# Kernel optimization log

Hardware: AMD Instinct MI355X
Metric: run time of the kernel (lower is better)

## Reference

```python
import jax, jax.numpy as jnp
import numpy as np

TEMP = 0.2
L_MAIN, L_VIEW, L_SUP, L_UNSUP = 1.0, 1.0, 1.0, 0.2
N, D, V, P, NEG, U = 100000, 256, 3, 1024, 1024, 2048


def setup_inputs() -> dict:
    key = jax.random.key(0)
    ks = jax.random.split(key, 8)
    fused_logit = jax.random.normal(ks[0], (N,), dtype=jnp.float32)
    view_logits = jax.random.normal(ks[1], (V, N), dtype=jnp.float32)
    proj = jax.random.normal(ks[2], (V, N, D), dtype=jnp.float32)
    proj = proj / jnp.linalg.norm(proj, axis=-1, keepdims=True)  # 'already normalized'
    labels = jax.random.randint(ks[3], (N,), 0, 2).astype(jnp.float32)
    train_mask = jax.random.randint(ks[4], (N,), 0, 2).astype(bool)
    train_pos_idx = jax.random.randint(ks[5], (P,), 0, N)
    train_neg_idx = jax.random.randint(ks[6], (NEG,), 0, N)
    unlabeled_idx = jax.random.randint(ks[7], (U,), 0, N)  # len == max_unsup_samples -> no subsampling
    return dict(fused_logit=fused_logit, view_logits=view_logits, proj=proj,
                labels=labels, train_mask=train_mask, train_pos_idx=train_pos_idx,
                train_neg_idx=train_neg_idx, unlabeled_idx=unlabeled_idx)


def _masked_bce(logits, labels, mask):
    # BCEWithLogitsLoss mean over masked elements (stable formulation)
    bce = jnp.maximum(logits, 0) - logits * labels + jnp.log1p(jnp.exp(-jnp.abs(logits)))
    mf = mask.astype(logits.dtype)
    return jnp.sum(bce * mf) / jnp.maximum(jnp.sum(mf), 1.0)


def _sup_contrastive(proj, pos_idx, neg_idx, temp):
    lab_idx = jnp.concatenate([pos_idx, neg_idx])
    node_labels = jnp.concatenate([jnp.ones(pos_idx.shape[0]), jnp.zeros(neg_idx.shape[0])])
    L = lab_idx.shape[0]
    Vv = proj.shape[0]
    z = proj[:, lab_idx, :].transpose(1, 0, 2)          # [L, V, D]
    zf = z.reshape(L * Vv, -1)                           # [L*V, D]
    sim = (zf @ zf.T) / temp                             # [L*V, L*V]
    sim = sim - jax.lax.stop_gradient(sim.max(axis=1, keepdims=True))
    es = jnp.exp(sim)
    node = jnp.repeat(jnp.arange(L), Vv)
    view = jnp.tile(jnp.arange(Vv), L)
    flab = jnp.repeat(node_labels, Vv)
    sn = node[:, None] == node[None, :]
    sv = view[:, None] == view[None, :]
    sl = flab[:, None] == flab[None, :]
    eye = jnp.eye(L * Vv, dtype=bool)
    pos_m = ((sn & ~sv) | (~sn & sl)) & ~eye
    neg_m = (~sn) & (~sl) & ~eye
    den_m = pos_m | neg_m
    denom = jnp.sum(es * den_m.astype(es.dtype), axis=1) + 1e-12
    posf = pos_m.astype(es.dtype)
    log_prob = -jnp.log((es * posf + 1e-12) / denom[:, None])
    pos_count = pos_m.sum(axis=1)
    loss_per_anchor = jnp.sum(log_prob * posf, axis=1) / (pos_count.astype(es.dtype) + 1e-12)
    valid = ((pos_count > 0) & (den_m.sum(axis=1) > 0)).astype(es.dtype)
    return jnp.sum(loss_per_anchor * valid) / jnp.maximum(jnp.sum(valid), 1.0)


def _unsup_consistency(proj, unl_idx, temp):
    # Vectorized form of the double python loop: full cosine-sim matrix with
    # masked denominator (all but self) and positives = same node, other views.
    Vv = proj.shape[0]
    z = proj[:, unl_idx, :].transpose(1, 0, 2)           # [U, V, D]
    Uu = z.shape[0]
    M = Uu * Vv
    zf = z.reshape(M, -1)
    zn = zf / (jnp.linalg.norm(zf, axis=1, keepdims=True) + 1e-8)
    es = jnp.exp((zn @ zn.T) / temp)                     # [M, M]
    denom = es.sum(axis=1) - jnp.diag(es) + 1e-12        # exclude self
    node = jnp.repeat(jnp.arange(Uu), Vv)
    view = jnp.tile(jnp.arange(Vv), Uu)
    pos_m = (node[:, None] == node[None, :]) & (view[:, None] != view[None, :])
    posf = pos_m.astype(es.dtype)
    log_prob = -jnp.log(es / denom[:, None])
    per_anchor = jnp.sum(log_prob * posf, axis=1) / (Vv - 1)
    return jnp.mean(per_anchor)


def reference(fused_logit, view_logits, proj, labels, train_mask,
              train_pos_idx, train_neg_idx, unlabeled_idx):
    main_loss = _masked_bce(fused_logit, labels, train_mask)
    view_loss = jnp.mean(jax.vmap(lambda lg: _masked_bce(lg, labels, train_mask))(view_logits))
    sup_loss = _sup_contrastive(proj, train_pos_idx, train_neg_idx, TEMP)
    unsup_loss = _unsup_consistency(proj, unlabeled_idx, TEMP)
    total = L_MAIN * main_loss + L_VIEW * view_loss + L_SUP * sup_loss + L_UNSUP * unsup_loss
    return jnp.stack([total, main_loss, view_loss, sup_loss, unsup_loss])
```

## Files before the change

### kernel.cpp

```cpp
#include <hip/hip_runtime.h>
#include <math.h>

typedef short short8 __attribute__((ext_vector_type(8)));
typedef float floatx4 __attribute__((ext_vector_type(4)));

#define TEMP_INV 5.0f
#define W_UNSUP 0.2f
#define NB_BCE 256
#define NSPLIT 8

static __device__ __forceinline__ unsigned short f2bf(float f) {
  unsigned int u = __float_as_uint(f);
  u += 0x7FFFu + ((u >> 16) & 1u);
  return (unsigned short)(u >> 16);
}

__device__ __forceinline__ float block_sum256(float v) {
  __shared__ float sh[4];
  for (int m = 1; m <= 32; m <<= 1) v += __shfl_xor(v, m);
  __syncthreads();
  if ((threadIdx.x & 63) == 0) sh[threadIdx.x >> 6] = v;
  __syncthreads();
  return sh[0] + sh[1] + sh[2] + sh[3];
}

__global__ void detect_kernel(const unsigned int* __restrict__ w, int nw, int* __restrict__ flag) {
  __shared__ int s_int, s_flt;
  if (threadIdx.x == 0) { s_int = 1; s_flt = 1; }
  __syncthreads();
  for (int i = threadIdx.x; i < nw; i += blockDim.x) {
    unsigned int x = w[i];
    if (x != 0u && x != 1u) s_int = 0;
    if (x != 0u && x != 0x3F800000u) s_flt = 0;
  }
  __syncthreads();
  if (threadIdx.x == 0) *flag = s_int ? 0 : (s_flt ? 1 : 2);
}

__global__ __launch_bounds__(256) void bce_kernel(
    const float* __restrict__ fused, const float* __restrict__ viewl,
    const float* __restrict__ labels, const void* __restrict__ maskp,
    const int* __restrict__ flagp, float* __restrict__ partials, int N, int V) {
  const int flag = *flagp;
  float cnt = 0.f, sm = 0.f;
  float sv[8];
  for (int v = 0; v < 8; v++) sv[v] = 0.f;
  const int Vc = V > 8 ? 8 : V;
  for (int i = blockIdx.x * blockDim.x + threadIdx.x; i < N; i += gridDim.x * blockDim.x) {
    bool m;
    if (flag == 0)      m = ((const int*)maskp)[i] != 0;
    else if (flag == 1) m = ((const float*)maskp)[i] != 0.0f;
    else                m = ((const unsigned char*)maskp)[i] != 0;
    if (!m) continue;
    float y = labels[i];
    cnt += 1.0f;
    float x = fused[i];
    sm += fmaxf(x, 0.f) - x * y + log1pf(__expf(-fabsf(x)));
    for (int v = 0; v < Vc; v++) {
      float xv = viewl[(size_t)v * N + i];
      sv[v] += fmaxf(xv, 0.f) - xv * y + log1pf(__expf(-fabsf(xv)));
    }
  }
  float tot = block_sum256(cnt);
  if (threadIdx.x == 0) partials[blockIdx.x * 16 + 0] = tot;
  tot = block_sum256(sm);
  if (threadIdx.x == 0) partials[blockIdx.x * 16 + 1] = tot;
  for (int v = 0; v < Vc; v++) {
    tot = block_sum256(sv[v]);
    if (threadIdx.x == 0) partials[blockIdx.x * 16 + 2 + v] = tot;
  }
}

__global__ __launch_bounds__(256) void gather_kernel(
    const float* __restrict__ proj, const int* __restrict__ pos_idx,
    const int* __restrict__ neg_idx, const int* __restrict__ unl_idx,
    unsigned short* __restrict__ zsup, unsigned short* __restrict__ zuns,
    float* __restrict__ dsup, float* __restrict__ duns,
    float* __restrict__ Esup, float* __restrict__ Bsup,
    float* __restrict__ Euns, float* __restrict__ Buns,
    int N, int D, int V, int P, int Msup, int Muns) {
  const int prob = blockIdx.y;
  const int M = prob ? Muns : Msup;
  const int r0 = blockIdx.x * 8;
  const int t = threadIdx.x;
  if (t < 8) {
    int rz = r0 + t;
    if (rz < M) {
      if (prob) { Euns[rz] = 0.f; Buns[rz] = 0.f; }
      else      { Esup[rz] = 0.f; Bsup[rz] = 0.f; }
    }
  }
  const int sub = t >> 5, ln = t & 31;
  const int r = r0 + sub;
  if (r >= M) return;
  const int l = r / V, v = r - l * V;
  const int idx = prob ? unl_idx[l] : (l < P ? pos_idx[l] : neg_idx[l - P]);
  const float* src = proj + ((size_t)v * N + (size_t)idx) * D + ln * 8;
  floatx4 p0 = *(const floatx4*)(src);
  floatx4 p1 = *(const floatx4*)(src + 4);
  float s = 0.f;
#pragma unroll
  for (int k = 0; k < 4; k++) s += p0[k] * p0[k] + p1[k] * p1[k];
  for (int m = 1; m <= 16; m <<= 1) s += __shfl_xor(s, m);
  const float n2 = s;
  float sc = 1.0f, dval = n2 * TEMP_INV;
  if (prob) {
    sc = 1.0f / (sqrtf(n2) + 1e-8f);
    dval = n2 * sc * sc * TEMP_INV;
  }
  short8 vv;
#pragma unroll
  for (int k = 0; k < 4; k++) {
    vv[k]     = (short)f2bf(p0[k] * sc);
    vv[k + 4] = (short)f2bf(p1[k] * sc);
  }
  unsigned short* zd = prob ? zuns : zsup;
  *(short8*)(zd + (size_t)r * 256 + ln * 8) = vv;
  if (ln == 0) (prob ? duns : dsup)[r] = dval;
}

__global__ __launch_bounds__(256) void sim_kernel(
    const unsigned short* __restrict__ zsup, const unsigned short* __restrict__ zuns,
    float* __restrict__ Esup, float* __restrict__ Bsup,
    float* __restrict__ Euns, float* __restrict__ Buns,
    int Msup, int Muns, int PV, int V, int nsSup, int nsUns) {
  const int prob = blockIdx.y;
  const unsigned short* __restrict__ z = prob ? zuns : zsup;
  float* __restrict__ Ep = prob ? Euns : Esup;
  float* __restrict__ Bp = prob ? Buns : Bsup;
  const int M = prob ? Muns : Msup;
  const int ns = prob ? nsUns : nsSup;

  const int si = blockIdx.x / NSPLIT;
  const int s  = blockIdx.x - si * NSPLIT;
  if (si >= ns) return;

  const int R0 = si * 64;
  const int tid = threadIdx.x;
  const int wave = tid >> 6;
  const int wr = wave >> 1, wc = wave & 1;
  const int q = (tid >> 4) & 3;
  const int n16 = tid & 15;

  __shared__ __align__(16) unsigned short lds[64 * 264];

  short8 a[2][8];
#pragma unroll
  for (int m = 0; m < 2; m++) {
    int row = R0 + wr * 32 + m * 16 + n16;
    if (row >= M) row = M - 1;
    const unsigned short* zr = z + (size_t)row * 256 + q * 8;
#pragma unroll
    for (int ks = 0; ks < 8; ks++) a[m][ks] = *(const short8*)(zr + ks * 32);
  }

  int bs[2][4], be[2][4];
#pragma unroll
  for (int m = 0; m < 2; m++)
#pragma unroll
    for (int r = 0; r < 4; r++) {
      int row = R0 + wr * 32 + m * 16 + q * 4 + r;
      if (row >= M) row = M - 1;
      if (prob == 0) { bs[m][r] = row < PV ? 0 : PV; be[m][r] = row < PV ? PV : M; }
      else           { int b0 = (row / V) * V; bs[m][r] = b0; be[m][r] = b0 + V; }
    }

  float er0[4] = {0, 0, 0, 0}, er1[4] = {0, 0, 0, 0};
  float br0[4] = {0, 0, 0, 0}, br1[4] = {0, 0, 0, 0};

  for (int tj = si + s; tj < ns; tj += NSPLIT) {
    const int C0 = tj * 64;
    __syncthreads();
#pragma unroll
    for (int cc = 0; cc < 8; cc++) {
      int chunk = cc * 256 + tid;
      int rrow = chunk >> 5;
      int off = (chunk & 31) * 8;
      int gcol = C0 + rrow;
      short8 vv = {0, 0, 0, 0, 0, 0, 0, 0};
      if (gcol < M) vv = *(const short8*)(z + (size_t)gcol * 256 + off);
      *(short8*)(&lds[rrow * 264 + off]) = vv;
    }
    __syncthreads();

    floatx4 acc00 = {0.f, 0.f, 0.f, 0.f}, acc01 = {0.f, 0.f, 0.f, 0.f};
    floatx4 acc10 = {0.f, 0.f, 0.f, 0.f}, acc11 = {0.f, 0.f, 0.f, 0.f};
#pragma unroll
    for (int ks = 0; ks < 8; ks++) {
      const unsigned short* bp = &lds[(wc * 32 + n16) * 264 + q * 8 + ks * 32];
      short8 b0 = *(const short8*)bp;
      short8 b1 = *(const short8*)(bp + 16 * 264);
      acc00 = __builtin_amdgcn_mfma_f32_16x16x32_bf16(a[0][ks], b0, acc00, 0, 0, 0);
      acc01 = __builtin_amdgcn_mfma_f32_16x16x32_bf16(a[0][ks], b1, acc01, 0, 0, 0);
      acc10 = __builtin_amdgcn_mfma_f32_16x16x32_bf16(a[1][ks], b0, acc10, 0, 0, 0);
      acc11 = __builtin_amdgcn_mfma_f32_16x16x32_bf16(a[1][ks], b1, acc11, 0, 0, 0);
    }

    float ec0 = 0.f, ec1 = 0.f, bc0 = 0.f, bc1 = 0.f;
    const int j0 = C0 + wc * 32 + n16;
    const int j1 = j0 + 16;

#define EPI(ACC, MM, JN, ECOL, BCOL, ERA, BRA)                        \
  _Pragma("unroll")                                                   \
  for (int r = 0; r < 4; r++) {                                       \
    int row = R0 + wr * 32 + MM * 16 + q * 4 + r;                     \
    float tv = ACC[r] * TEMP_INV;                                     \
    bool valid = (row < M) && (JN < M);                               \
    float e = valid ? __expf(tv - 5.0f) : 0.0f;                       \
    float bv = (valid && JN >= bs[MM][r] && JN < be[MM][r]) ? tv : 0.0f; \
    ERA[r] += e; BRA[r] += bv; ECOL += e; BCOL += bv;                 \
  }
    EPI(acc00, 0, j0, ec0, bc0, er0, br0)
    EPI(acc01, 0, j1, ec1, bc1, er0, br0)
    EPI(acc10, 1, j0, ec0, bc0, er1, br1)
    EPI(acc11, 1, j1, ec1, bc1, er1, br1)
#undef EPI

    if (tj != si) {
      float e = ec0, b = bc0;
      e += __shfl_xor(e, 16); e += __shfl_xor(e, 32);
      b += __shfl_xor(b, 16); b += __shfl_xor(b, 32);
      if (q == 0 && j0 < M) { atomicAdd(&Ep[j0], e); atomicAdd(&Bp[j0], b); }
      e = ec1; b = bc1;
      e += __shfl_xor(e, 16); e += __shfl_xor(e, 32);
      b += __shfl_xor(b, 16); b += __shfl_xor(b, 32);
      if (q == 0 && j1 < M) { atomicAdd(&Ep[j1], e); atomicAdd(&Bp[j1], b); }
    }
  }

#pragma unroll
  for (int mr = 0; mr < 8; mr++) {
    const int m = mr >> 2, r = mr & 3;
    float e = m ? er1[r] : er0[r];
    float b = m ? br1[r] : br0[r];
    for (int msk = 1; msk <= 8; msk <<= 1) { e += __shfl_xor(e, msk); b += __shfl_xor(b, msk); }
    int row = R0 + wr * 32 + m * 16 + q * 4 + r;
    if (n16 == 0 && row < M) {
      atomicAdd(&Ep[row], e);
      atomicAdd(&Bp[row], b);
    }
  }
}

__global__ __launch_bounds__(256) void finalize_kernel(
    const float* __restrict__ partials,
    const float* __restrict__ Esup, const float* __restrict__ Bsup, const float* __restrict__ dsup,
    const float* __restrict__ Euns, const float* __restrict__ Buns, const float* __restrict__ duns,
    int Msup, int Muns, int PV, int P, int NEG, int V, float* __restrict__ out) {
  const int t = threadIdx.x;
  float cnt = 0.f, sm = 0.f, sv[8];
  for (int v = 0; v < 8; v++) sv[v] = 0.f;
  const int Vc = V > 8 ? 8 : V;
  for (int b = t; b < NB_BCE; b += 256) {
    cnt += partials[b * 16 + 0];
    sm  += partials[b * 16 + 1];
    for (int v = 0; v < Vc; v++) sv[v] += partials[b * 16 + 2 + v];
  }
  cnt = block_sum256(cnt);
  sm = block_sum256(sm);
  float svt = 0.f;
  for (int v = 0; v < Vc; v++) svt += block_sum256(sv[v]);
  const float denomC = fmaxf(cnt, 1.0f);
  const float main_loss = sm / denomC;
  const float view_loss = (svt / denomC) / (float)V;

  float ssup = 0.f;
  for (int row = t; row < Msup; row += 256) {
    float E = Esup[row], B = Bsup[row];
    float d = dsup[row];
    float dn = E - __expf(d - 5.0f);
    float cl = (row < PV) ? (float)P : (float)NEG;
    float pc = (float)(V - 1) + (cl - 1.0f) * (float)V;
    ssup += logf(dn) + 5.0f - (B - d) / pc;
  }
  ssup = block_sum256(ssup);
  const float sup_loss = ssup / (float)Msup;

  float suns = 0.f;
  for (int row = t; row < Muns; row += 256) {
    float E = Euns[row], B = Buns[row];
    float d = duns[row];
    float dn = E - __expf(d - 5.0f);
    suns += logf(dn) + 5.0f - (B - d) / (float)(V - 1);
  }
  suns = block_sum256(suns);
  const float unsup_loss = suns / (float)Muns;

  if (t == 0) {
    float total = main_loss + view_loss + sup_loss + W_UNSUP * unsup_loss;
    out[0] = total;
    out[1] = main_loss;
    out[2] = view_loss;
    out[3] = sup_loss;
    out[4] = unsup_loss;
  }
}

extern "C" void kernel_launch(void* const* d_in, const int* in_sizes, int n_in,
                              void* d_out, int out_size, void* d_ws, size_t ws_size,
                              hipStream_t stream) {
  const float* fused  = (const float*)d_in[0];
  const float* viewl  = (const float*)d_in[1];
  const float* proj   = (const float*)d_in[2];
  const float* labels = (const float*)d_in[3];
  const void*  maskp  = d_in[4];
  const int* pos_idx  = (const int*)d_in[5];
  const int* neg_idx  = (const int*)d_in[6];
  const int* unl_idx  = (const int*)d_in[7];

  const int N = in_sizes[0];
  const int V = in_sizes[1] / N;
  const int D = in_sizes[2] / in_sizes[1];
  const int P = in_sizes[5];
  const int NEG = in_sizes[6];
  const int U = in_sizes[7];
  const int L = P + NEG;
  const int Msup = L * V;
  const int Muns = U * V;
  const int PV = P * V;

  char* ws = (char*)d_ws;
  size_t off = 0;
  auto alloc = [&](size_t bytes) { size_t o = off; off += (bytes + 255) & ~(size_t)255; return o; };
  const size_t o_flag = alloc(4);
  const size_t o_part = alloc((size_t)NB_BCE * 16 * 4);
  const size_t o_zsup = alloc((size_t)Msup * D * 2);
  const size_t o_zuns = alloc((size_t)Muns * D * 2);
  const size_t o_dsup = alloc((size_t)Msup * 4);
  const size_t o_duns = alloc((size_t)Muns * 4);
  const size_t o_Esup = alloc((size_t)Msup * 4);
  const size_t o_Bsup = alloc((size_t)Msup * 4);
  const size_t o_Euns = alloc((size_t)Muns * 4);
  const size_t o_Buns = alloc((size_t)Muns * 4);

  int* flag = (int*)(ws + o_flag);
  float* partials = (float*)(ws + o_part);
  unsigned short* zsup = (unsigned short*)(ws + o_zsup);
  unsigned short* zuns = (unsigned short*)(ws + o_zuns);
  float* dsup = (float*)(ws + o_dsup);
  float* duns = (float*)(ws + o_duns);
  float* Esup = (float*)(ws + o_Esup);
  float* Bsup = (float*)(ws + o_Bsup);
  float* Euns = (float*)(ws + o_Euns);
  float* Buns = (float*)(ws + o_Buns);

  int nw = N / 4 < 256 ? N / 4 : 256;
  detect_kernel<<<1, 256, 0, stream>>>((const unsigned int*)maskp, nw, flag);
  bce_kernel<<<NB_BCE, 256, 0, stream>>>(fused, viewl, labels, maskp, flag, partials, N, V);

  const int Mmax = Msup > Muns ? Msup : Muns;
  dim3 ggrid((Mmax + 7) / 8, 2);
  gather_kernel<<<ggrid, 256, 0, stream>>>(proj, pos_idx, neg_idx, unl_idx,
                                           zsup, zuns, dsup, duns,
                                           Esup, Bsup, Euns, Buns,
                                           N, D, V, P, Msup, Muns);

  const int nsS = (Msup + 63) / 64;
  const int nsU = (Muns + 63) / 64;
  const int nsMax = nsS > nsU ? nsS : nsU;
  dim3 sgrid(nsMax * NSPLIT, 2);
  sim_kernel<<<sgrid, 256, 0, stream>>>(zsup, zuns, Esup, Bsup, Euns, Buns,
                                        Msup, Muns, PV, V, nsS, nsU);

  finalize_kernel<<<1, 256, 0, stream>>>(partials, Esup, Bsup, dsup, Euns, Buns, duns,
                                         Msup, Muns, PV, P, NEG, V, (float*)d_out);
}
```

Baseline: 463.4 us.

## Prefetch next sim tile into registers and fold mask detection into BCE kernel

The sim kernel now loads the next 64-column tile of z into registers while the current tile is written to LDS and consumed, so global load latency overlaps the MFMA work. The separate single-block detect kernel is removed; every BCE block now redoes the mask-dtype detection itself, saving one launch and the serial dependency. The cost is extra register pressure from the eight prefetch vectors, and redundant detection reads in each BCE block.

```diff
diff --git a/kernel.cpp b/kernel.cpp
--- a/kernel.cpp
+++ b/kernel.cpp
@@ -24,29 +24,33 @@
   return sh[0] + sh[1] + sh[2] + sh[3];
 }
 
-__global__ void detect_kernel(const unsigned int* __restrict__ w, int nw, int* __restrict__ flag) {
-  __shared__ int s_int, s_flt;
-  if (threadIdx.x == 0) { s_int = 1; s_flt = 1; }
-  __syncthreads();
-  for (int i = threadIdx.x; i < nw; i += blockDim.x) {
-    unsigned int x = w[i];
-    if (x != 0u && x != 1u) s_int = 0;
-    if (x != 0u && x != 0x3F800000u) s_flt = 0;
-  }
-  __syncthreads();
-  if (threadIdx.x == 0) *flag = s_int ? 0 : (s_flt ? 1 : 2);
-}
-
 __global__ __launch_bounds__(256) void bce_kernel(
     const float* __restrict__ fused, const float* __restrict__ viewl,
     const float* __restrict__ labels, const void* __restrict__ maskp,
-    const int* __restrict__ flagp, float* __restrict__ partials, int N, int V) {
-  const int flag = *flagp;
+    float* __restrict__ partials, int N, int V, int nw) {
+  __shared__ int s_int, s_flt;
+  const int t = threadIdx.x;
+  if (t == 0) { s_int = 1; s_flt = 1; }
+  __syncthreads();
+  {
+    const unsigned int* w = (const unsigned int*)maskp;
+    int okI = 1, okF = 1;
+    for (int i = t; i < nw; i += 256) {
+      unsigned int x = w[i];
+      if (x != 0u && x != 1u) okI = 0;
+      if (x != 0u && x != 0x3F800000u) okF = 0;
+    }
+    if (!okI) atomicAnd(&s_int, 0);
+    if (!okF) atomicAnd(&s_flt, 0);
+  }
+  __syncthreads();
+  const int flag = s_int ? 0 : (s_flt ? 1 : 2);
+
   float cnt = 0.f, sm = 0.f;
   float sv[8];
   for (int v = 0; v < 8; v++) sv[v] = 0.f;
   const int Vc = V > 8 ? 8 : V;
-  for (int i = blockIdx.x * blockDim.x + threadIdx.x; i < N; i += gridDim.x * blockDim.x) {
+  for (int i = blockIdx.x * blockDim.x + t; i < N; i += gridDim.x * blockDim.x) {
     bool m;
     if (flag == 0)      m = ((const int*)maskp)[i] != 0;
     else if (flag == 1) m = ((const float*)maskp)[i] != 0.0f;
@@ -62,12 +66,12 @@
     }
   }
   float tot = block_sum256(cnt);
-  if (threadIdx.x == 0) partials[blockIdx.x * 16 + 0] = tot;
+  if (t == 0) partials[blockIdx.x * 16 + 0] = tot;
   tot = block_sum256(sm);
-  if (threadIdx.x == 0) partials[blockIdx.x * 16 + 1] = tot;
+  if (t == 0) partials[blockIdx.x * 16 + 1] = tot;
   for (int v = 0; v < Vc; v++) {
     tot = block_sum256(sv[v]);
-    if (threadIdx.x == 0) partials[blockIdx.x * 16 + 2 + v] = tot;
+    if (t == 0) partials[blockIdx.x * 16 + 2 + v] = tot;
   }
 }
 
@@ -144,6 +148,9 @@
 
   __shared__ __align__(16) unsigned short lds[64 * 264];
 
+  const int srow = tid >> 5;
+  const int soff = (tid & 31) * 8;
+
   short8 a[2][8];
 #pragma unroll
   for (int m = 0; m < 2; m++) {
@@ -168,18 +175,37 @@
   float er0[4] = {0, 0, 0, 0}, er1[4] = {0, 0, 0, 0};
   float br0[4] = {0, 0, 0, 0}, br1[4] = {0, 0, 0, 0};
 
-  for (int tj = si + s; tj < ns; tj += NSPLIT) {
+  short8 cur[8];
+  int tj = si + s;
+  if (tj < ns) {
+    const int C0 = tj * 64;
+#pragma unroll
+    for (int cc = 0; cc < 8; cc++) {
+      int gcol = C0 + srow + cc * 8;
+      short8 vv = {0, 0, 0, 0, 0, 0, 0, 0};
+      if (gcol < M) vv = *(const short8*)(z + (size_t)gcol * 256 + soff);
+      cur[cc] = vv;
+    }
+  }
+
+  for (; tj < ns; tj += NSPLIT) {
     const int C0 = tj * 64;
     __syncthreads();
 #pragma unroll
-    for (int cc = 0; cc < 8; cc++) {
-      int chunk = cc * 256 + tid;
-      int rrow = chunk >> 5;
-      int off = (chunk & 31) * 8;
-      int gcol = C0 + rrow;
-      short8 vv = {0, 0, 0, 0, 0, 0, 0, 0};
-      if (gcol < M) vv = *(const short8*)(z + (size_t)gcol * 256 + off);
-      *(short8*)(&lds[rrow * 264 + off]) = vv;
+    for (int cc = 0; cc < 8; cc++)
+      *(short8*)(&lds[(srow + cc * 8) * 264 + soff]) = cur[cc];
+    {
+      int tjn = tj + NSPLIT;
+      if (tjn < ns) {
+        const int C0n = tjn * 64;
+#pragma unroll
+        for (int cc = 0; cc < 8; cc++) {
+          int gcol = C0n + srow + cc * 8;
+          short8 vv = {0, 0, 0, 0, 0, 0, 0, 0};
+          if (gcol < M) vv = *(const short8*)(z + (size_t)gcol * 256 + soff);
+          cur[cc] = vv;
+        }
+      }
     }
     __syncthreads();
 
@@ -322,7 +348,6 @@
   char* ws = (char*)d_ws;
   size_t off = 0;
   auto alloc = [&](size_t bytes) { size_t o = off; off += (bytes + 255) & ~(size_t)255; return o; };
-  const size_t o_flag = alloc(4);
   const size_t o_part = alloc((size_t)NB_BCE * 16 * 4);
   const size_t o_zsup = alloc((size_t)Msup * D * 2);
   const size_t o_zuns = alloc((size_t)Muns * D * 2);
@@ -333,7 +358,6 @@
   const size_t o_Euns = alloc((size_t)Muns * 4);
   const size_t o_Buns = alloc((size_t)Muns * 4);
 
-  int* flag = (int*)(ws + o_flag);
   float* partials = (float*)(ws + o_part);
   unsigned short* zsup = (unsigned short*)(ws + o_zsup);
   unsigned short* zuns = (unsigned short*)(ws + o_zuns);
@@ -345,8 +369,7 @@
   float* Buns = (float*)(ws + o_Buns);
 
   int nw = N / 4 < 256 ? N / 4 : 256;
-  detect_kernel<<<1, 256, 0, stream>>>((const unsigned int*)maskp, nw, flag);
-  bce_kernel<<<NB_BCE, 256, 0, stream>>>(fused, viewl, labels, maskp, flag, partials, N, V);
+  bce_kernel<<<NB_BCE, 256, 0, stream>>>(fused, viewl, labels, maskp, partials, N, V, nw);
 
   const int Mmax = Msup > Muns ? Msup : Muns;
   dim3 ggrid((Mmax + 7) / 8, 2);
```

Result: faster. 445.3 us (-3.9%).
